# Kernel optimization log

Hardware: AMD Instinct MI355X
Metric: run time of the kernel (lower is better)

The kernel has to match this reference:

```python
import jax, jax.numpy as jnp
import numpy as np

NHEAD = 16
D_MODEL = 1024
DK = D_MODEL // NHEAD
Q_DIM = V_DIM = K_DIM = 1024
B, S = 2, 2048


def _xavier(key, shape):
    # xavier_uniform over last two dims (fan_in=shape[-2], fan_out=shape[-1])
    fan_in, fan_out = shape[-2], shape[-1]
    limit = float(np.sqrt(6.0 / (fan_in + fan_out)))
    return jax.random.uniform(key, shape, jnp.float32, -limit, limit)


def setup_inputs() -> dict:
    key = jax.random.key(0)
    kq, kv, kk, kwq, kwv, kwk = jax.random.split(key, 6)
    q = jax.random.normal(kq, (B, S, Q_DIM), jnp.float32)
    v = jax.random.normal(kv, (B, S, V_DIM), jnp.float32)
    k = jax.random.normal(kk, (B, S, K_DIM), jnp.float32)
    # causal mask: True = attend, matches masked_fill(~mask, -inf)
    causal = jnp.tril(jnp.ones((S, S), dtype=bool))
    attn_mask = jnp.broadcast_to(causal, (B, S, S))
    q_proj_mats = _xavier(kwq, (NHEAD, Q_DIM, DK))
    v_proj_mats = _xavier(kwv, (NHEAD, V_DIM, DK))
    k_proj_mats = _xavier(kwk, (NHEAD, K_DIM, DK))
    return {"q": q, "v": v, "k": k, "attn_mask": attn_mask,
            "q_proj_mats": q_proj_mats, "v_proj_mats": v_proj_mats,
            "k_proj_mats": k_proj_mats}


def reference(q, v, k, attn_mask, q_proj_mats, v_proj_mats, k_proj_mats):
    bsz, seq_len, _ = q.shape
    # per-head projections: [B,S,dim] x [H,dim,dk] -> [B,H,S,dk]
    qp = jnp.einsum('bsk,hkd->bhsd', q, q_proj_mats)
    vp = jnp.einsum('bsk,hkd->bhsd', v, v_proj_mats)
    kp = jnp.einsum('bsk,hkd->bhsd', k, k_proj_mats)
    # NOTE: original scales by sqrt(d_model), not sqrt(dk)
    scale = 1.0 / jnp.sqrt(jnp.float32(D_MODEL))
    logits = jnp.einsum('bhqd,bhkd->bhqk', qp, kp) * scale  # [B,H,S,S]
    logits = jnp.where(attn_mask[:, None, :, :], logits, -jnp.inf)
    score = jax.nn.softmax(logits, axis=-1)
    weighted = jnp.einsum('bhkd,bhqk->bqhd', vp, score)  # [B,S,H,dk]
    return weighted.reshape(bsz, seq_len, -1)
```

## Files before the change

kernel.cpp:

```cpp
#include <hip/hip_runtime.h>
#include <cstdint>
#include <cstddef>

#define NB 2
#define NS 2048
#define NH 16
#define NDK 64
#define NDM 1024
#define SCALE 0.03125f
#define QSCALE 0.045084220f

using u16 = unsigned short;
typedef __attribute__((ext_vector_type(8))) short bf16x8;
typedef __attribute__((ext_vector_type(4))) short bf16x4;
typedef __attribute__((ext_vector_type(4))) float f32x4;

#define AS1 __attribute__((address_space(1)))
#define AS3 __attribute__((address_space(3)))

__device__ __forceinline__ u16 f2bf(float f) {
    unsigned int x = __float_as_uint(f);
    return (u16)((x + 0x7FFFu + ((x >> 16) & 1u)) >> 16);
}
__device__ __forceinline__ unsigned int packbf(float f0, float f1) {
    return __builtin_amdgcn_perm(__float_as_uint(f1), __float_as_uint(f0),
                                 0x07060302u);
}
__device__ __forceinline__ float fexp2(float x) {
#if defined(__HIP_DEVICE_COMPILE__) && __has_builtin(__builtin_amdgcn_exp2f)
    return __builtin_amdgcn_exp2f(x);
#else
    return __builtin_exp2f(x);
#endif
}
__device__ __forceinline__ f32x4 mfma16(bf16x4 a, bf16x4 b, f32x4 c) {
#if !defined(__HIP_DEVICE_COMPILE__)
    (void)a; (void)b;
    return c;
#elif __has_builtin(__builtin_amdgcn_mfma_f32_16x16x16bf16_1k)
    return __builtin_amdgcn_mfma_f32_16x16x16bf16_1k(a, b, c, 0, 0, 0);
#else
    typedef __attribute__((ext_vector_type(4))) __bf16 bf16v4;
    return __builtin_amdgcn_mfma_f32_16x16x16_bf16(
        *reinterpret_cast<bf16v4*>(&a), *reinterpret_cast<bf16v4*>(&b),
        c, 0, 0, 0);
#endif
}

__global__ __launch_bounds__(256)
void prep(const float* __restrict__ q, const float* __restrict__ v,
          const float* __restrict__ kkk,
          const float* __restrict__ qw, const float* __restrict__ vw,
          const float* __restrict__ kw,
          u16* __restrict__ xt, u16* __restrict__ wbt, int nxblk)
{
    __shared__ __align__(16) u16 SH[64 * 72];
    const int t = threadIdx.x;
    const int bid = blockIdx.x;
    if (bid < nxblk) {
        int z   = bid >> 7;
        int rem = bid & 127;
        int mt  = rem >> 2;
        int kq  = rem & 3;
        const float* X = (z == 0) ? q : (z == 1) ? v : kkk;
        const float* src = X + (size_t)mt * 128 * NDM;
        u16* dst = xt + (((size_t)z * 32 + mt) << 17);
        const int row = t >> 3;
        const int cl  = (t & 7) * 4;
        const int pl  = (t & 7) >> 1;
        const int hf  = (t & 1) * 4;
        for (int kk = kq * 8; kk < kq * 8 + 8; ++kk) {
            #pragma unroll
            for (int i = 0; i < 4; ++i) {
                int ml = row + 32 * i;
                float4 f = *reinterpret_cast<const float4*>(
                    src + (size_t)ml * NDM + kk * 32 + cl);
                uint2 u;
                u.x = packbf(f.x, f.y);
                u.y = packbf(f.z, f.w);
                *reinterpret_cast<uint2*>(&SH[(pl * 128 + ml) * 8 + hf]) = u;
            }
            __syncthreads();
            {
                uint4 o0 = *reinterpret_cast<uint4*>(&SH[(2 * t) * 8]);
                uint4 o1 = *reinterpret_cast<uint4*>(&SH[(2 * t + 1) * 8]);
                u16* dd = dst + ((size_t)kk << 12) + 2 * t * 8;
                *reinterpret_cast<uint4*>(dd)     = o0;
                *reinterpret_cast<uint4*>(dd + 8) = o1;
            }
            __syncthreads();
        }
    } else {
        int b  = bid - nxblk;
        int z  = b >> 8;
        int h  = (b >> 4) & 15;
        int k0 = (b & 15) * 64;
        const float* W = ((z == 0) ? qw : (z == 1) ? vw : kw)
                         + (size_t)h * NDM * NDK;
        {
            int kr = t >> 2, d0 = (t & 3) * 16;
            const float* src = W + (size_t)(k0 + kr) * NDK + d0;
            #pragma unroll
            for (int c = 0; c < 4; ++c) {
                float4 f = *reinterpret_cast<const float4*>(src + c * 4);
                SH[(d0 + c * 4 + 0) * 72 + kr] = f2bf(f.x);
                SH[(d0 + c * 4 + 1) * 72 + kr] = f2bf(f.y);
                SH[(d0 + c * 4 + 2) * 72 + kr] = f2bf(f.z);
                SH[(d0 + c * 4 + 3) * 72 + kr] = f2bf(f.w);
            }
        }
        __syncthreads();
        {
            int pl = t >> 6, d = t & 63;
            int nt = h >> 1;
            int cb = pl * 128 + (h & 1) * 64 + d;
            #pragma unroll
            for (int ki = 0; ki < 2; ++ki) {
                uint4 val = *reinterpret_cast<const uint4*>(
                    &SH[d * 72 + ki * 32 + pl * 8]);
                size_t base = (((size_t)z * 8 + nt) * 32 + (k0 >> 5) + ki) << 12;
                *reinterpret_cast<uint4*>(wbt + base + cb * 8) = val;
            }
        }
    }
}

__device__ __forceinline__ void gemm_epilogue(
    f32x4 acc[4][4], int z, int m0, int n0, int wm, int wn,
    int quad, int l15, u16* __restrict__ O)
{
    const int bb = m0 >> 11;
    const int hh = (n0 + wn) >> 6;
    const size_t headT = ((size_t)(bb * NH + hh)) << 17;
    if (z == 2) {
        #pragma unroll
        for (int mi = 0; mi < 4; ++mi) {
            #pragma unroll
            for (int r = 0; r < 4; ++r) {
                int s = (m0 + wm + mi * 16 + quad * 4 + r) & 2047;
                size_t tb = headT + ((size_t)(s >> 6) << 12) + (s & 63) * 8 + (l15 & 7);
                int chb = l15 >> 3;
                #pragma unroll
                for (int ni = 0; ni < 4; ++ni)
                    O[tb + (ni * 2 + chb) * 512] = f2bf(acc[mi][ni][r]);
            }
        }
    } else if (z == 1) {
        #pragma unroll
        for (int mi = 0; mi < 4; ++mi) {
            #pragma unroll
            for (int r = 0; r < 4; ++r) {
                int s = (m0 + wm + mi * 16 + quad * 4 + r) & 2047;
                size_t tb = headT + ((size_t)(s >> 6) << 12)
                          + ((s & 63) >> 3) * 512 + (s & 7);
                #pragma unroll
                for (int ni = 0; ni < 4; ++ni)
                    O[tb + (ni * 16 + l15) * 8] = f2bf(acc[mi][ni][r]);
            }
        }
    } else {
        #pragma unroll
        for (int mi = 0; mi < 4; ++mi) {
            #pragma unroll
            for (int r = 0; r < 4; ++r) {
                int s = (m0 + wm + mi * 16 + quad * 4 + r) & 2047;
                size_t rb = ((size_t)(bb * NH + hh) * NS + s) * NDK;
                #pragma unroll
                for (int ni = 0; ni < 4; ++ni)
                    O[rb + ni * 16 + l15] = f2bf(acc[mi][ni][r] * QSCALE);
            }
        }
    }
}

#define GSTEP(KK, CUR, NXT, PRE, VMA, DO_B, DO_A)                              \
    {                                                                          \
        asm volatile("s_waitcnt vmcnt(" #VMA ")" ::: "memory");                \
        __builtin_amdgcn_s_barrier();                                          \
        __builtin_amdgcn_sched_barrier(0);                                     \
        if (DO_B) {                                                            \
            const u16* bsrc_ = Bs + ((size_t)((KK) + 1) << 12)                 \
                             + (quad * 128 + wn + l15) * 8;                    \
            _Pragma("unroll")                                                  \
            for (int ni_ = 0; ni_ < 4; ++ni_)                                  \
                breg[NXT][ni_] = *reinterpret_cast<const bf16x8*>(             \
                    bsrc_ + ni_ * 128);                                        \
        }                                                                      \
        if (DO_A) {                                                            \
            const size_t off_ = (size_t)((KK) + 2) << 12;                      \
            _Pragma("unroll")                                                  \
            for (int i_ = 0; i_ < 2; ++i_) {                                   \
                int c_ = i_ * 256 + t;                                         \
                __builtin_amdgcn_global_load_lds(                              \
                    (const AS1 void*)(As + off_ + c_ * 8),                     \
                    (AS3 void*)&SA[PRE][c_ * 8], 16, 0, 0);                    \
            }                                                                  \
        }                                                                      \
        __builtin_amdgcn_sched_barrier(0);                                     \
        bf16x8 af_[4];                                                         \
        _Pragma("unroll")                                                      \
        for (int mi_ = 0; mi_ < 4; ++mi_)                                      \
            af_[mi_] = *reinterpret_cast<const bf16x8*>(                       \
                &SA[CUR][quad * 1024 + (wm + mi_ * 16 + l15) * 8]);            \
        _Pragma("unroll")                                                      \
        for (int mi_ = 0; mi_ < 4; ++mi_)                                      \
            _Pragma("unroll")                                                  \
            for (int ni_ = 0; ni_ < 4; ++ni_)                                  \
                acc[mi_][ni_] = __builtin_amdgcn_mfma_f32_16x16x32_bf16(       \
                    af_[mi_], breg[CUR][ni_], acc[mi_][ni_], 0, 0, 0);         \
    }

__global__ __launch_bounds__(256, 3)
void gemm_xt(const u16* __restrict__ xt, const u16* __restrict__ wbt,
             u16* __restrict__ qp, u16* __restrict__ vp,
             u16* __restrict__ kp)
{
    __shared__ __align__(16) u16 SA[3][4096];

    const int t    = threadIdx.x;
    const int lane = t & 63;
    const int w    = t >> 6;
    const int quad = lane >> 4, l15 = lane & 15;
    const int mt = blockIdx.x, nt = blockIdx.y, z = blockIdx.z;

    const u16* As = xt + (((size_t)z * 32 + mt) << 17);
    const u16* Bs = wbt + (((size_t)z * 8 + nt) << 17);
    u16* O = (z == 0) ? qp : (z == 1) ? vp : kp;
    const int wm = (w & 1) * 64, wn = (w >> 1) * 64;

    bf16x8 breg[3][4];

    #pragma unroll
    for (int i = 0; i < 2; ++i) {
        int c = i * 256 + t;
        __builtin_amdgcn_global_load_lds((const AS1 void*)(As + c * 8),
                                         (AS3 void*)&SA[0][c * 8], 16, 0, 0);
    }
    {
        const u16* bsrc = Bs + (quad * 128 + wn + l15) * 8;
        #pragma unroll
        for (int ni = 0; ni < 4; ++ni)
            breg[0][ni] = *reinterpret_cast<const bf16x8*>(bsrc + ni * 128);
    }
    #pragma unroll
    for (int i = 0; i < 2; ++i) {
        int c = i * 256 + t;
        __builtin_amdgcn_global_load_lds((const AS1 void*)(As + 4096 + c * 8),
                                         (AS3 void*)&SA[1][c * 8], 16, 0, 0);
    }

    f32x4 acc[4][4] = {};

    for (int kk = 0; kk < 30; kk += 3) {
        GSTEP(kk + 0, 0, 1, 2, 6, true, true);
        GSTEP(kk + 1, 1, 2, 0, 6, true, true);
        GSTEP(kk + 2, 2, 0, 1, 6, true, true);
    }
    GSTEP(30, 0, 1, 2, 6, true, false);
    GSTEP(31, 1, 2, 0, 4, false, false);

    gemm_epilogue(acc, z, mt * 128, nt * 128, wm, wn, quad, l15, O);
}
#undef GSTEP

__global__ __launch_bounds__(256)
void gemm_pack(const float* __restrict__ q, const float* __restrict__ v,
               const float* __restrict__ kkk, const u16* __restrict__ wbt,
               u16* __restrict__ qp, u16* __restrict__ vp,
               u16* __restrict__ kp)
{
    __shared__ __align__(16) u16 SA[2][4096];
    __shared__ __align__(16) u16 SB[2][4096];

    const int t    = threadIdx.x;
    const int lane = t & 63;
    const int w    = t >> 6;
    const int quad = lane >> 4, l15 = lane & 15;
    const int m0 = blockIdx.x * 128;
    const int n0 = blockIdx.y * 128;
    const int z  = blockIdx.z;

    const float* X = (z == 0) ? q : (z == 1) ? v : kkk;
    const u16* Wb2 = wbt + (((size_t)z * 8 + (n0 >> 7)) << 17);
    u16* O = (z == 0) ? qp : (z == 1) ? vp : kp;

    const int wm = (w & 1) * 64, wn = (w >> 1) * 64;
    const int arow = t >> 3;
    const int acol = (t & 7) * 4;
    const int apl  = (t & 7) >> 1;
    const int aj   = (t & 1) * 4;
    const float* xa = X + (size_t)(m0 + arow) * NDM + acol;

    float4 fA[4];
    #pragma unroll
    for (int i = 0; i < 4; ++i)
        fA[i] = *reinterpret_cast<const float4*>(xa + (size_t)(32 * i) * NDM);
    #pragma unroll
    for (int i = 0; i < 2; ++i) {
        int c = i * 256 + t;
        __builtin_amdgcn_global_load_lds((const AS1 void*)(Wb2 + c * 8),
                                         (AS3 void*)&SB[0][c * 8], 16, 0, 0);
    }

    f32x4 acc[4][4] = {};

    #pragma unroll 2
    for (int kk = 0; kk < 32; ++kk) {
        const int cur = kk & 1;
        #pragma unroll
        for (int i = 0; i < 4; ++i) {
            uint2 u;
            u.x = packbf(fA[i].x, fA[i].y);
            u.y = packbf(fA[i].z, fA[i].w);
            *reinterpret_cast<uint2*>(
                &SA[cur][apl * 1024 + (arow + 32 * i) * 8 + aj]) = u;
        }
        __syncthreads();

        if (kk < 31) {
            const int kn = (kk + 1) * 32;
            const float* p = xa + kn;
            #pragma unroll
            for (int i = 0; i < 4; ++i)
                fA[i] = *reinterpret_cast<const float4*>(p + (size_t)(32 * i) * NDM);
            const u16* src = Wb2 + ((size_t)(kk + 1) << 12);
            #pragma unroll
            for (int i = 0; i < 2; ++i) {
                int c = i * 256 + t;
                __builtin_amdgcn_global_load_lds((const AS1 void*)(src + c * 8),
                                                 (AS3 void*)&SB[cur ^ 1][c * 8], 16, 0, 0);
            }
        }

        bf16x8 af[4], bfr[4];
        #pragma unroll
        for (int mi = 0; mi < 4; ++mi)
            af[mi] = *reinterpret_cast<const bf16x8*>(
                &SA[cur][quad * 1024 + (wm + mi * 16 + l15) * 8]);
        #pragma unroll
        for (int ni = 0; ni < 4; ++ni)
            bfr[ni] = *reinterpret_cast<const bf16x8*>(
                &SB[cur][quad * 1024 + (wn + ni * 16 + l15) * 8]);
        #pragma unroll
        for (int mi = 0; mi < 4; ++mi)
            #pragma unroll
            for (int ni = 0; ni < 4; ++ni)
                acc[mi][ni] = __builtin_amdgcn_mfma_f32_16x16x32_bf16(
                    af[mi], bfr[ni], acc[mi][ni], 0, 0, 0);
    }

    gemm_epilogue(acc, z, m0, n0, wm, wn, quad, l15, O);
}

__global__ __launch_bounds__(256, 3)
void attn_kernel(const u16* __restrict__ QP, const u16* __restrict__ KP,
                 const u16* __restrict__ VT, float* __restrict__ Out)
{
    __shared__ __align__(16) u16 SMEM[16384];
    __shared__ float LS[4][4][16];

    u16* KB = SMEM;
    u16* VB = SMEM + 8192;

    const int t    = threadIdx.x;
    const int w    = t >> 6;
    const int lane = t & 63;
    const int quad = lane >> 4, l15 = lane & 15;

    const int qt = 31 - (blockIdx.x >> 5);
    const int bh = blockIdx.x & 31;
    const size_t headQ = (size_t)bh * NS * NDK;
    const size_t headT = (size_t)bh << 17;
    const int q0 = qt * 64;

    bf16x8 qf[4][2];
    #pragma unroll
    for (int qg = 0; qg < 4; ++qg) {
        const u16* qa = QP + headQ + (size_t)(q0 + qg * 16 + l15) * NDK + quad * 8;
        qf[qg][0] = *reinterpret_cast<const bf16x8*>(qa);
        qf[qg][1] = *reinterpret_cast<const bf16x8*>(qa + 32);
    }

    f32x4 o[4][4] = {};
    float ls[4] = {};

    #pragma unroll
    for (int i = 0; i < 2; ++i) {
        int c = i * 256 + t;
        __builtin_amdgcn_global_load_lds((const AS1 void*)(KP + headT + c * 8),
                                         (AS3 void*)&KB[c * 8], 16, 0, 0);
        __builtin_amdgcn_global_load_lds((const AS1 void*)(VT + headT + c * 8),
                                         (AS3 void*)&VB[c * 8], 16, 0, 0);
    }

    for (int kt = 0; kt <= qt; ++kt) {
        const int cur = kt & 1;
        __syncthreads();
        if (kt < qt) {
            const size_t tb = headT + ((size_t)(kt + 1) << 12);
            const int nb = cur ^ 1;
            #pragma unroll
            for (int i = 0; i < 2; ++i) {
                int c = i * 256 + t;
                __builtin_amdgcn_global_load_lds((const AS1 void*)(KP + tb + c * 8),
                                                 (AS3 void*)&KB[nb * 4096 + c * 8], 16, 0, 0);
                __builtin_amdgcn_global_load_lds((const AS1 void*)(VT + tb + c * 8),
                                                 (AS3 void*)&VB[nb * 4096 + c * 8], 16, 0, 0);
            }
        }
        const u16* KBc = KB + cur * 4096;
        const u16* VBc = VB + cur * 4096;

        bf16x8 k0 = *reinterpret_cast<const bf16x8*>(
            &KBc[quad * 512 + (w * 16 + l15) * 8]);
        bf16x8 k1 = *reinterpret_cast<const bf16x8*>(
            &KBc[(quad + 4) * 512 + (w * 16 + l15) * 8]);

        const bool diag = (kt == qt);
        bf16x4 pf[4];
        #pragma unroll
        for (int qg = 0; qg < 4; ++qg) {
            f32x4 z = {};
            f32x4 s = __builtin_amdgcn_mfma_f32_16x16x32_bf16(k1, qf[qg][1],
                        __builtin_amdgcn_mfma_f32_16x16x32_bf16(k0, qf[qg][0], z, 0, 0, 0),
                        0, 0, 0);
            float p0 = fexp2(s[0]);
            float p1 = fexp2(s[1]);
            float p2 = fexp2(s[2]);
            float p3 = fexp2(s[3]);
            if (diag) {
                const int kb = w * 16 + quad * 4;
                const int qr = qg * 16 + l15;
                if (kb + 0 > qr) p0 = 0.0f;
                if (kb + 1 > qr) p1 = 0.0f;
                if (kb + 2 > qr) p2 = 0.0f;
                if (kb + 3 > qr) p3 = 0.0f;
            }
            ls[qg] += (p0 + p1) + (p2 + p3);
            union { unsigned int u[2]; bf16x4 v; } pu;
            pu.u[0] = packbf(p0, p1);
            pu.u[1] = packbf(p2, p3);
            pf[qg] = pu.v;
        }

        #pragma unroll
        for (int d = 0; d < 4; ++d) {
            const bf16x4 vf = *reinterpret_cast<const bf16x4*>(
                &VBc[(2 * w + (quad >> 1)) * 512 + (d * 16 + l15) * 8 + (quad & 1) * 4]);
            #pragma unroll
            for (int qg = 0; qg < 4; ++qg)
                o[qg][d] = mfma16(pf[qg], vf, o[qg][d]);
        }
    }

    #pragma unroll
    for (int qg = 0; qg < 4; ++qg) {
        ls[qg] += __shfl_xor(ls[qg], 16, 64);
        ls[qg] += __shfl_xor(ls[qg], 32, 64);
    }

    __syncthreads();
    if (quad == 0) {
        #pragma unroll
        for (int qg = 0; qg < 4; ++qg) LS[w][qg][l15] = ls[qg];
    }
    __syncthreads();
    float inv[4];
    #pragma unroll
    for (int qg = 0; qg < 4; ++qg)
        inv[qg] = 1.0f / (LS[0][qg][l15] + LS[1][qg][l15]
                        + LS[2][qg][l15] + LS[3][qg][l15]);

    float* SC = reinterpret_cast<float*>(SMEM);
    const int bb = bh >> 4, h = bh & 15;
    #pragma unroll
    for (int round = 0; round < 2; ++round) {
        const int qgA = round * 2, qgB = round * 2 + 1;
        if (w != qgA) {
            #pragma unroll
            for (int d = 0; d < 4; ++d)
                *reinterpret_cast<f32x4*>(
                    SC + ((qgA & 1) * 4 + w) * 1024 + (d * 16 + l15) * 16 + quad * 4)
                    = o[qgA][d];
        }
        if (w != qgB) {
            #pragma unroll
            for (int d = 0; d < 4; ++d)
                *reinterpret_cast<f32x4*>(
                    SC + ((qgB & 1) * 4 + w) * 1024 + (d * 16 + l15) * 16 + quad * 4)
                    = o[qgB][d];
        }
        __syncthreads();
        if (w == qgA || w == qgB) {
            const int qg = w;
            const float invq = (w == qgA) ? inv[qgA] : inv[qgB];
            f32x4 acc[4];
            #pragma unroll
            for (int d = 0; d < 4; ++d) {
                acc[d] = (w == qgA) ? o[qgA][d] : o[qgB][d];
                #pragma unroll
                for (int w2 = 0; w2 < 4; ++w2) {
                    if (w2 != qg)
                        acc[d] += *reinterpret_cast<const f32x4*>(
                            SC + ((qg & 1) * 4 + w2) * 1024
                               + (d * 16 + l15) * 16 + quad * 4);
                }
            }
            #pragma unroll
            for (int r = 0; r < 4; ++r) {
                const float iv = __shfl(invq, quad * 4 + r, 64);
                const size_t ob = ((size_t)bb * NS + q0 + qg * 16 + quad * 4 + r)
                                  * NDM + h * 64 + l15;
                #pragma unroll
                for (int d = 0; d < 4; ++d)
                    Out[ob + d * 16] = acc[d][r] * iv;
            }
        }
        if (round == 0) __syncthreads();
    }
}

extern "C" void kernel_launch(void* const* d_in, const int* in_sizes, int n_in,
                              void* d_out, int out_size, void* d_ws, size_t ws_size,
                              hipStream_t stream) {
    const float* q  = (const float*)d_in[0];
    const float* v  = (const float*)d_in[1];
    const float* k  = (const float*)d_in[2];
    const float* qw = (const float*)d_in[4];
    const float* vw = (const float*)d_in[5];
    const float* kw = (const float*)d_in[6];

    const size_t PSZ = (size_t)NB * NH * NS * NDK;
    u16* wbt = (u16*)d_ws;
    u16* qp  = wbt + (size_t)3 * NDM * NDM;
    u16* vp  = qp + PSZ;
    u16* kp  = vp + PSZ;
    u16* xt  = kp + PSZ;

    const size_t NEED_XT = ((size_t)3 * NDM * NDM + 3 * PSZ
                            + (size_t)3 * 4096 * NDM) * 2;
    const bool xtpath = (ws_size >= NEED_XT);
    const int nx = xtpath ? 384 : 0;

    prep<<<dim3(768 + nx), dim3(256), 0, stream>>>(
        q, v, k, qw, vw, kw, xtpath ? xt : (u16*)d_ws, wbt, nx);

    if (xtpath)
        gemm_xt<<<dim3(32, 8, 3), dim3(256), 0, stream>>>(xt, wbt, qp, vp, kp);
    else
        gemm_pack<<<dim3(32, 8, 3), dim3(256), 0, stream>>>(q, v, k, wbt,
                                                            qp, vp, kp);

    attn_kernel<<<dim3(32 * 32), dim3(256), 0, stream>>>(qp, kp, vp,
                                                         (float*)d_out);
}
```

Measured before the change: 190.6 us.

## Triple-buffer K tiles in LDS and stream V fragments directly into registers

The attention loop now keeps K tiles in a three-slot LDS ring, prefetched two tiles ahead. V fragments are loaded straight from global memory into rotating registers instead of being staged through LDS. The loop is unrolled by three with explicit vmcnt waits and raw barriers in place of __syncthreads. The epilogue scratch layout is compacted to fit the smaller shared allocation. The aim is to cut LDS traffic and footprint and hide load latency better, at the cost of more VGPRs, uncoalesced-style per-lane V loads, and fragile manual wait counting.

```diff
diff --git a/kernel.cpp b/kernel.cpp
--- a/kernel.cpp
+++ b/kernel.cpp
@@ -352,15 +352,85 @@
     gemm_epilogue(acc, z, m0, n0, wm, wn, quad, l15, O);
 }
 
+#define ATTN_COMPUTE(KBC, VRC, DIAG)                                           \
+    {                                                                          \
+        const u16* KBc_ = KBs[KBC];                                            \
+        bf16x8 k0_ = *reinterpret_cast<const bf16x8*>(                         \
+            &KBc_[quad * 512 + (w * 16 + l15) * 8]);                           \
+        bf16x8 k1_ = *reinterpret_cast<const bf16x8*>(                         \
+            &KBc_[(quad + 4) * 512 + (w * 16 + l15) * 8]);                     \
+        bf16x4 pf_[4];                                                         \
+        _Pragma("unroll")                                                      \
+        for (int qg_ = 0; qg_ < 4; ++qg_) {                                    \
+            f32x4 z_ = {};                                                     \
+            f32x4 s_ = __builtin_amdgcn_mfma_f32_16x16x32_bf16(k1_, qf[qg_][1],\
+                __builtin_amdgcn_mfma_f32_16x16x32_bf16(k0_, qf[qg_][0], z_,   \
+                                                        0, 0, 0), 0, 0, 0);    \
+            float p0_ = fexp2(s_[0]);                                          \
+            float p1_ = fexp2(s_[1]);                                          \
+            float p2_ = fexp2(s_[2]);                                          \
+            float p3_ = fexp2(s_[3]);                                          \
+            if (DIAG) {                                                        \
+                const int kb_ = w * 16 + quad * 4;                             \
+                const int qr_ = qg_ * 16 + l15;                                \
+                if (kb_ + 0 > qr_) p0_ = 0.0f;                                 \
+                if (kb_ + 1 > qr_) p1_ = 0.0f;                                 \
+                if (kb_ + 2 > qr_) p2_ = 0.0f;                                 \
+                if (kb_ + 3 > qr_) p3_ = 0.0f;                                 \
+            }                                                                  \
+            ls[qg_] += (p0_ + p1_) + (p2_ + p3_);                              \
+            union { unsigned int u[2]; bf16x4 v; } pu_;                        \
+            pu_.u[0] = packbf(p0_, p1_);                                       \
+            pu_.u[1] = packbf(p2_, p3_);                                       \
+            pf_[qg_] = pu_.v;                                                  \
+        }                                                                      \
+        _Pragma("unroll")                                                      \
+        for (int d_ = 0; d_ < 4; ++d_) {                                       \
+            _Pragma("unroll")                                                  \
+            for (int qg_ = 0; qg_ < 4; ++qg_)                                  \
+                o[qg_][d_] = mfma16(pf_[qg_], VRC[d_], o[qg_][d_]);            \
+        }                                                                      \
+    }
+
+#define ATTN_STEP(KT, KBC, VRC, KBP, VRN)                                      \
+    {                                                                          \
+        asm volatile("s_waitcnt vmcnt(2)" ::: "memory");                       \
+        __builtin_amdgcn_s_barrier();                                          \
+        __builtin_amdgcn_sched_barrier(0);                                     \
+        {                                                                      \
+            const u16* vsrc_ = Vbase + (size_t)((KT) + 1) * 4096;              \
+            _Pragma("unroll")                                                  \
+            for (int d_ = 0; d_ < 4; ++d_)                                     \
+                VRN[d_] = *reinterpret_cast<const bf16x4*>(vsrc_ + d_ * 128);  \
+        }                                                                      \
+        if ((KT) + 2 <= qt) {                                                  \
+            const size_t ko_ = headT + ((size_t)((KT) + 2) << 12);             \
+            _Pragma("unroll")                                                  \
+            for (int i_ = 0; i_ < 2; ++i_) {                                   \
+                int c_ = i_ * 256 + t;                                         \
+                __builtin_amdgcn_global_load_lds(                              \
+                    (const AS1 void*)(KP + ko_ + c_ * 8),                      \
+                    (AS3 void*)&KBs[KBP][c_ * 8], 16, 0, 0);                   \
+            }                                                                  \
+        }                                                                      \
+        __builtin_amdgcn_sched_barrier(0);                                     \
+        ATTN_COMPUTE(KBC, VRC, false);                                         \
+    }
+
+#define ATTN_FIN(KT, KBC, VRC)                                                 \
+    {                                                                          \
+        asm volatile("s_waitcnt vmcnt(0)" ::: "memory");                       \
+        __builtin_amdgcn_s_barrier();                                          \
+        __builtin_amdgcn_sched_barrier(0);                                     \
+        ATTN_COMPUTE(KBC, VRC, true);                                          \
+    }
+
 __global__ __launch_bounds__(256, 3)
 void attn_kernel(const u16* __restrict__ QP, const u16* __restrict__ KP,
                  const u16* __restrict__ VT, float* __restrict__ Out)
 {
-    __shared__ __align__(16) u16 SMEM[16384];
+    __shared__ __align__(16) u16 KBs[3][4096];
     __shared__ float LS[4][4][16];
-
-    u16* KB = SMEM;
-    u16* VB = SMEM + 8192;
 
     const int t    = threadIdx.x;
     const int w    = t >> 6;
@@ -383,73 +453,47 @@
 
     f32x4 o[4][4] = {};
     float ls[4] = {};
+    bf16x4 vr0[4], vr1[4], vr2[4];
+
+    const u16* Vbase = VT + headT + (2 * w + (quad >> 1)) * 512
+                     + l15 * 8 + (quad & 1) * 4;
 
     #pragma unroll
     for (int i = 0; i < 2; ++i) {
         int c = i * 256 + t;
         __builtin_amdgcn_global_load_lds((const AS1 void*)(KP + headT + c * 8),
-                                         (AS3 void*)&KB[c * 8], 16, 0, 0);
-        __builtin_amdgcn_global_load_lds((const AS1 void*)(VT + headT + c * 8),
-                                         (AS3 void*)&VB[c * 8], 16, 0, 0);
-    }
-
-    for (int kt = 0; kt <= qt; ++kt) {
-        const int cur = kt & 1;
-        __syncthreads();
-        if (kt < qt) {
-            const size_t tb = headT + ((size_t)(kt + 1) << 12);
-            const int nb = cur ^ 1;
-            #pragma unroll
-            for (int i = 0; i < 2; ++i) {
-                int c = i * 256 + t;
-                __builtin_amdgcn_global_load_lds((const AS1 void*)(KP + tb + c * 8),
-                                                 (AS3 void*)&KB[nb * 4096 + c * 8], 16, 0, 0);
-                __builtin_amdgcn_global_load_lds((const AS1 void*)(VT + tb + c * 8),
-                                                 (AS3 void*)&VB[nb * 4096 + c * 8], 16, 0, 0);
-            }
-        }
-        const u16* KBc = KB + cur * 4096;
-        const u16* VBc = VB + cur * 4096;
-
-        bf16x8 k0 = *reinterpret_cast<const bf16x8*>(
-            &KBc[quad * 512 + (w * 16 + l15) * 8]);
-        bf16x8 k1 = *reinterpret_cast<const bf16x8*>(
-            &KBc[(quad + 4) * 512 + (w * 16 + l15) * 8]);
-
-        const bool diag = (kt == qt);
-        bf16x4 pf[4];
-        #pragma unroll
-        for (int qg = 0; qg < 4; ++qg) {
-            f32x4 z = {};
-            f32x4 s = __builtin_amdgcn_mfma_f32_16x16x32_bf16(k1, qf[qg][1],
-                        __builtin_amdgcn_mfma_f32_16x16x32_bf16(k0, qf[qg][0], z, 0, 0, 0),
-                        0, 0, 0);
-            float p0 = fexp2(s[0]);
-            float p1 = fexp2(s[1]);
-            float p2 = fexp2(s[2]);
-            float p3 = fexp2(s[3]);
-            if (diag) {
-                const int kb = w * 16 + quad * 4;
-                const int qr = qg * 16 + l15;
-                if (kb + 0 > qr) p0 = 0.0f;
-                if (kb + 1 > qr) p1 = 0.0f;
-                if (kb + 2 > qr) p2 = 0.0f;
-                if (kb + 3 > qr) p3 = 0.0f;
-            }
-            ls[qg] += (p0 + p1) + (p2 + p3);
-            union { unsigned int u[2]; bf16x4 v; } pu;
-            pu.u[0] = packbf(p0, p1);
-            pu.u[1] = packbf(p2, p3);
-            pf[qg] = pu.v;
-        }
-
-        #pragma unroll
-        for (int d = 0; d < 4; ++d) {
-            const bf16x4 vf = *reinterpret_cast<const bf16x4*>(
-                &VBc[(2 * w + (quad >> 1)) * 512 + (d * 16 + l15) * 8 + (quad & 1) * 4]);
-            #pragma unroll
-            for (int qg = 0; qg < 4; ++qg)
-                o[qg][d] = mfma16(pf[qg], vf, o[qg][d]);
+                                         (AS3 void*)&KBs[0][c * 8], 16, 0, 0);
+    }
+    #pragma unroll
+    for (int d = 0; d < 4; ++d)
+        vr0[d] = *reinterpret_cast<const bf16x4*>(Vbase + d * 128);
+    if (qt >= 1) {
+        #pragma unroll
+        for (int i = 0; i < 2; ++i) {
+            int c = i * 256 + t;
+            __builtin_amdgcn_global_load_lds(
+                (const AS1 void*)(KP + headT + 4096 + c * 8),
+                (AS3 void*)&KBs[1][c * 8], 16, 0, 0);
+        }
+    }
+
+    int kt = 0;
+    for (; kt + 3 <= qt; kt += 3) {
+        ATTN_STEP(kt + 0, 0, vr0, 2, vr1);
+        ATTN_STEP(kt + 1, 1, vr1, 0, vr2);
+        ATTN_STEP(kt + 2, 2, vr2, 1, vr0);
+    }
+    {
+        const int rem = qt - kt;
+        if (rem == 0) {
+            ATTN_FIN(kt, 0, vr0);
+        } else if (rem == 1) {
+            ATTN_STEP(kt, 0, vr0, 2, vr1);
+            ATTN_FIN(kt + 1, 1, vr1);
+        } else {
+            ATTN_STEP(kt, 0, vr0, 2, vr1);
+            ATTN_STEP(kt + 1, 1, vr1, 0, vr2);
+            ATTN_FIN(kt + 2, 2, vr2);
         }
     }
 
@@ -471,40 +515,41 @@
         inv[qg] = 1.0f / (LS[0][qg][l15] + LS[1][qg][l15]
                         + LS[2][qg][l15] + LS[3][qg][l15]);
 
-    float* SC = reinterpret_cast<float*>(SMEM);
+    float* SC = reinterpret_cast<float*>(KBs);
     const int bb = bh >> 4, h = bh & 15;
     #pragma unroll
     for (int round = 0; round < 2; ++round) {
         const int qgA = round * 2, qgB = round * 2 + 1;
         if (w != qgA) {
+            const int slot = (w < qgA) ? w : (w - 1);
             #pragma unroll
             for (int d = 0; d < 4; ++d)
                 *reinterpret_cast<f32x4*>(
-                    SC + ((qgA & 1) * 4 + w) * 1024 + (d * 16 + l15) * 16 + quad * 4)
+                    SC + slot * 1024 + (d * 16 + l15) * 16 + quad * 4)
                     = o[qgA][d];
         }
         if (w != qgB) {
+            const int slot = 3 + ((w < qgB) ? w : (w - 1));
             #pragma unroll
             for (int d = 0; d < 4; ++d)
                 *reinterpret_cast<f32x4*>(
-                    SC + ((qgB & 1) * 4 + w) * 1024 + (d * 16 + l15) * 16 + quad * 4)
+                    SC + slot * 1024 + (d * 16 + l15) * 16 + quad * 4)
                     = o[qgB][d];
         }
         __syncthreads();
         if (w == qgA || w == qgB) {
             const int qg = w;
+            const int sbase = (w == qgA) ? 0 : 3;
             const float invq = (w == qgA) ? inv[qgA] : inv[qgB];
             f32x4 acc[4];
             #pragma unroll
             for (int d = 0; d < 4; ++d) {
                 acc[d] = (w == qgA) ? o[qgA][d] : o[qgB][d];
                 #pragma unroll
-                for (int w2 = 0; w2 < 4; ++w2) {
-                    if (w2 != qg)
-                        acc[d] += *reinterpret_cast<const f32x4*>(
-                            SC + ((qg & 1) * 4 + w2) * 1024
-                               + (d * 16 + l15) * 16 + quad * 4);
-                }
+                for (int s2 = 0; s2 < 3; ++s2)
+                    acc[d] += *reinterpret_cast<const f32x4*>(
+                        SC + (sbase + s2) * 1024
+                           + (d * 16 + l15) * 16 + quad * 4);
             }
             #pragma unroll
             for (int r = 0; r < 4; ++r) {
@@ -519,6 +564,9 @@
         if (round == 0) __syncthreads();
     }
 }
+#undef ATTN_STEP
+#undef ATTN_FIN
+#undef ATTN_COMPUTE
 
 extern "C" void kernel_launch(void* const* d_in, const int* in_sizes, int n_in,
                               void* d_out, int out_size, void* d_ws, size_t ws_size,
```

Measured after the change: 318.1 us. 66.8% more time.
